# Kernel optimization log

Measured on AMD Instinct MI355X. Metric: run time of the kernel, lower is better.

The kernel has to match this reference:

```python
import jax, jax.numpy as jnp
import numpy as np

SCALE = 8.0  # sqrt(d_head=64)
NEG = -1e9


def setup_inputs() -> dict:
    key = jax.random.key(0)
    kq, kk, kv, km = jax.random.split(key, 4)
    B, H, S, D = 2, 16, 2048, 64
    q = jax.random.normal(kq, (B, H, S, D), dtype=jnp.float32)
    k = jax.random.normal(kk, (B, H, S, D), dtype=jnp.float32)
    v = jax.random.normal(kv, (B, H, S, D), dtype=jnp.float32)
    mask = jax.random.randint(km, (B, 1, 1, S), 0, 2, dtype=jnp.int32)
    return {"q": q, "k": k, "v": v, "mask": mask}


def reference(q, k, v, mask):
    # scores: [B,H,S,S]
    scores = jnp.einsum("bhqd,bhkd->bhqk", q / SCALE, k)
    scores = jnp.where(mask == 0, NEG, scores)
    attn = jax.nn.softmax(scores, axis=-1)  # dropout p=0 -> identity
    out = jnp.einsum("bhqk,bhkd->bhqd", attn, v)
    return (out, attn)
```

## Files before the change

### kernel.cpp

```cpp
#include <hip/hip_runtime.h>
#include <hip/hip_bf16.h>


#define S_LEN 2048
#define DH 64
#define QT 128
#define NCH (S_LEN / 64)

typedef __attribute__((ext_vector_type(8))) short  s16x8;
typedef __attribute__((ext_vector_type(4))) short  s16x4;
typedef __attribute__((ext_vector_type(8))) __bf16 bf16x8;
typedef __attribute__((ext_vector_type(4))) float  f32x4;
typedef __attribute__((ext_vector_type(2))) unsigned int u32x2;

__device__ __forceinline__ short f2bf(float x) {
    __hip_bfloat16 h = __float2bfloat16(x);
    return *reinterpret_cast<short*>(&h);
}
__device__ __forceinline__ unsigned pack2(float a, float b) {
    return (unsigned)(unsigned short)f2bf(a) | ((unsigned)(unsigned short)f2bf(b) << 16);
}
__device__ __forceinline__ bf16x8 ldfrag(const short* p) {
    s16x8 t = *(const s16x8*)p;
    return __builtin_bit_cast(bf16x8, t);
}
__device__ __forceinline__ int SW (int r, int c) { return r * 64 + (c ^ ((r & 7) << 3)); }
__device__ __forceinline__ int SWF(int r, int c) { return r * 64 + (c ^ ((r & 7) << 3)); }

__global__ __launch_bounds__(512, 4) void sdpa_kernel(
    const float* __restrict__ q, const float* __restrict__ k,
    const float* __restrict__ v, const int* __restrict__ mask,
    float* __restrict__ out, float* __restrict__ attn)
{
    __shared__ __align__(16) short shK[2][64 * 64];
    __shared__ __align__(16) short shVt[2][64 * 64];
    __shared__ __align__(16) float shPT[8][16 * 64];
    __shared__ char shMask[S_LEN];

    const int tid  = threadIdx.x;
    const int lane = tid & 63;
    const int w    = tid >> 6;
    const int l15  = lane & 15;
    const int lg   = lane >> 4;

    const int bh = blockIdx.y;
    const int q0 = blockIdx.x * QT;
    const int b  = bh >> 4;

    const float* qbase = q + ((size_t)bh * S_LEN + q0) * DH;
    const float* kbase = k + (size_t)bh * S_LEN * DH;
    const float* vbase = v + (size_t)bh * S_LEN * DH;
    float* attnbh = attn + (size_t)bh * S_LEN * S_LEN;

    for (int i = tid; i < S_LEN; i += 512)
        shMask[i] = (char)(mask[b * S_LEN + i] != 0);

    const int qrow = w * 16 + l15;
    bf16x8 qf0, qf1;
    {
        const float* qp = qbase + qrow * DH + 8 * lg;
        const float4 a0 = *(const float4*)(qp);
        const float4 a1 = *(const float4*)(qp + 4);
        const float4 b0 = *(const float4*)(qp + 32);
        const float4 b1 = *(const float4*)(qp + 36);
        s16x8 t0, t1;
        t0[0]=f2bf(a0.x*0.125f); t0[1]=f2bf(a0.y*0.125f); t0[2]=f2bf(a0.z*0.125f); t0[3]=f2bf(a0.w*0.125f);
        t0[4]=f2bf(a1.x*0.125f); t0[5]=f2bf(a1.y*0.125f); t0[6]=f2bf(a1.z*0.125f); t0[7]=f2bf(a1.w*0.125f);
        t1[0]=f2bf(b0.x*0.125f); t1[1]=f2bf(b0.y*0.125f); t1[2]=f2bf(b0.z*0.125f); t1[3]=f2bf(b0.w*0.125f);
        t1[4]=f2bf(b1.x*0.125f); t1[5]=f2bf(b1.y*0.125f); t1[6]=f2bf(b1.z*0.125f); t1[7]=f2bf(b1.w*0.125f);
        qf0 = __builtin_bit_cast(bf16x8, t0);
        qf1 = __builtin_bit_cast(bf16x8, t1);
    }

    const int krow = tid >> 3;
    const int kd0  = (tid & 7) * 8;
    auto loadK = [&](int c0, float4& a, float4& bb) {
        const float* src = kbase + (size_t)(c0 + krow) * DH + kd0;
        a  = *(const float4*)(src);
        bb = *(const float4*)(src + 4);
    };
    auto writeK = [&](short* dst, const float4& a, const float4& bb) {
        s16x8 vv;
        vv[0]=f2bf(a.x);  vv[1]=f2bf(a.y);  vv[2]=f2bf(a.z);  vv[3]=f2bf(a.w);
        vv[4]=f2bf(bb.x); vv[5]=f2bf(bb.y); vv[6]=f2bf(bb.z); vv[7]=f2bf(bb.w);
        *(s16x8*)&dst[SW(krow, kd0)] = vv;
    };
    const int vr0 = (tid & 31) * 2;
    const int vdg = tid >> 5;
    auto loadV = [&](int c0, float4& a, float4& bb) {
        const float* src = vbase + (size_t)(c0 + vr0) * DH + vdg * 4;
        a  = *(const float4*)(src);
        bb = *(const float4*)(src + DH);
    };
    auto writeVt = [&](short* dst, const float4& a, const float4& bb) {
        const float av[4] = {a.x, a.y, a.z, a.w};
        const float bv[4] = {bb.x, bb.y, bb.z, bb.w};
        int* dw = (int*)dst;
#pragma unroll
        for (int i = 0; i < 4; ++i) {
            const int d = vdg * 4 + i;
            dw[(d * 64 + (vr0 ^ ((d & 7) << 3))) >> 1] = (int)pack2(av[i], bv[i]);
        }
    };

    float4 ka, kb;
    loadK(0, ka, kb);
    writeK(shK[0], ka, kb);
    __syncthreads();

    float lacc = 0.f;
    for (int t = 0; t < NCH; ++t) {
        const int cur = t & 1;
        if (t + 1 < NCH) loadK((t + 1) * 64, ka, kb);
        __syncthreads();
        const short* K = shK[cur];
        const int c0 = t * 64;
        f32x4 s[4] = {{0,0,0,0},{0,0,0,0},{0,0,0,0},{0,0,0,0}};
#pragma unroll
        for (int ct = 0; ct < 4; ++ct) {
            const int kc = ct * 16 + l15;
            bf16x8 kf = ldfrag(&K[SW(kc, 8 * lg)]);
            s[ct] = __builtin_amdgcn_mfma_f32_16x16x32_bf16(kf, qf0, s[ct], 0, 0, 0);
            kf = ldfrag(&K[SW(kc, 32 + 8 * lg)]);
            s[ct] = __builtin_amdgcn_mfma_f32_16x16x32_bf16(kf, qf1, s[ct], 0, 0, 0);
        }
#pragma unroll
        for (int ct = 0; ct < 4; ++ct) {
            const unsigned mw = *(const unsigned*)&shMask[c0 + ct * 16 + lg * 4];
#pragma unroll
            for (int r = 0; r < 4; ++r)
                lacc += ((mw >> (8 * r)) & 1u) ? __expf(s[ct][r]) : 0.f;
        }
        if (t + 1 < NCH) writeK(shK[cur ^ 1], ka, kb);
    }
    lacc += __shfl_xor(lacc, 16);
    lacc += __shfl_xor(lacc, 32);
    const float lnInvl = -__logf(lacc);

    f32x4 oacc[4] = {{0,0,0,0},{0,0,0,0},{0,0,0,0},{0,0,0,0}};
    float4 va, vb;
    loadK(0, ka, kb);
    loadV(0, va, vb);
    writeK(shK[0], ka, kb);
    writeVt(shVt[0], va, vb);

    float* const shPTw = shPT[w];
    for (int t = 0; t < NCH; ++t) {
        const int cur = t & 1;
        if (t + 1 < NCH) { loadK((t + 1) * 64, ka, kb); loadV((t + 1) * 64, va, vb); }
        __syncthreads();
        const short* K  = shK[cur];
        const short* Vt = shVt[cur];
        const int c0 = t * 64;

        f32x4 s[4] = {{0,0,0,0},{0,0,0,0},{0,0,0,0},{0,0,0,0}};
#pragma unroll
        for (int ct = 0; ct < 4; ++ct) {
            const int kc = ct * 16 + l15;
            bf16x8 kf = ldfrag(&K[SW(kc, 8 * lg)]);
            s[ct] = __builtin_amdgcn_mfma_f32_16x16x32_bf16(kf, qf0, s[ct], 0, 0, 0);
            kf = ldfrag(&K[SW(kc, 32 + 8 * lg)]);
            s[ct] = __builtin_amdgcn_mfma_f32_16x16x32_bf16(kf, qf1, s[ct], 0, 0, 0);
        }
        s16x4 pf[4];
#pragma unroll
        for (int ct = 0; ct < 4; ++ct) {
            const unsigned mw = *(const unsigned*)&shMask[c0 + ct * 16 + lg * 4];
            f32x4 p;
#pragma unroll
            for (int r = 0; r < 4; ++r)
                p[r] = ((mw >> (8 * r)) & 1u) ? __expf(s[ct][r] + lnInvl) : 0.f;
            *(f32x4*)&shPTw[SWF(l15, ct * 16 + lg * 4)] = p;
            u32x2 pk;
            pk[0] = pack2(p[0], p[1]);
            pk[1] = pack2(p[2], p[3]);
            pf[ct] = __builtin_bit_cast(s16x4, pk);
        }
#pragma unroll
        for (int st = 0; st < 4; ++st) {
            const int rowIdx = (lane >> 3) + (st >> 1) * 8;
            const int cm     = (lane & 7) * 4 + (st & 1) * 32;
            const f32x4 pv_ = *(const f32x4*)&shPTw[SWF(rowIdx, cm)];
            __builtin_nontemporal_store(
                pv_, (f32x4*)(attnbh + (size_t)(q0 + w * 16 + rowIdx) * S_LEN + c0 + cm));
        }
#pragma unroll
        for (int dt = 0; dt < 4; ++dt) {
#pragma unroll
            for (int ct = 0; ct < 4; ++ct) {
                const s16x4 af = *(const s16x4*)&Vt[SW(dt * 16 + l15, ct * 16 + 4 * lg)];
                oacc[dt] = __builtin_amdgcn_mfma_f32_16x16x16bf16_1k(af, pf[ct], oacc[dt], 0, 0, 0);
            }
        }
        if (t + 1 < NCH) { writeK(shK[cur ^ 1], ka, kb); writeVt(shVt[cur ^ 1], va, vb); }
    }

    float* obase = out + ((size_t)bh * S_LEN + q0 + qrow) * DH;
#pragma unroll
    for (int dt = 0; dt < 4; ++dt)
        __builtin_nontemporal_store(oacc[dt], (f32x4*)(obase + dt * 16 + lg * 4));
}

extern "C" void kernel_launch(void* const* d_in, const int* in_sizes, int n_in,
                              void* d_out, int out_size, void* d_ws, size_t ws_size,
                              hipStream_t stream)
{
    const float* q    = (const float*)d_in[0];
    const float* k    = (const float*)d_in[1];
    const float* v    = (const float*)d_in[2];
    const int*   mask = (const int*)d_in[3];
    float* out  = (float*)d_out;
    float* attn = out + (size_t)2 * 16 * 2048 * 64;

    dim3 grid(S_LEN / QT, 2 * 16);
    sdpa_kernel<<<grid, dim3(512), 0, stream>>>(q, k, v, mask, out, attn);
}
```

Baseline: 168.5 us.

## Widen normalizer pass to 128-key chunks and reorder main-loop staging

The first pass, which computes the softmax denominator, now processes 128 keys per iteration. It uses wider K loads, four split accumulators and half as many barriers, with K kept in a shared-memory arena that the second pass also reuses. In the second pass, the next K/V tile is written to shared memory and the PV MFMAs are issued before the attention-matrix stores. This aims to overlap global stores with compute and to drop one barrier on the first iteration. The row sums are passed through shPT with an extra block barrier. The wider loads add register pressure under the 512-thread, 4-block launch bound.

```diff
diff --git a/kernel.cpp b/kernel.cpp
--- a/kernel.cpp
+++ b/kernel.cpp
@@ -6,6 +6,7 @@
 #define DH 64
 #define QT 128
 #define NCH (S_LEN / 64)
+#define NCHA (S_LEN / 128)
 
 typedef __attribute__((ext_vector_type(8))) short  s16x8;
 typedef __attribute__((ext_vector_type(4))) short  s16x4;
@@ -32,8 +33,7 @@
     const float* __restrict__ v, const int* __restrict__ mask,
     float* __restrict__ out, float* __restrict__ attn)
 {
-    __shared__ __align__(16) short shK[2][64 * 64];
-    __shared__ __align__(16) short shVt[2][64 * 64];
+    __shared__ __align__(16) char  arena[32 * 1024];
     __shared__ __align__(16) float shPT[8][16 * 64];
     __shared__ char shMask[S_LEN];
 
@@ -72,29 +72,90 @@
         qf1 = __builtin_bit_cast(bf16x8, t1);
     }
 
+    {
+        const int krow2 = tid >> 2;
+        const int kd2   = (tid & 3) * 16;
+        float4 k0_, k1_, k2_, k3_;
+        auto loadK2 = [&](int c0) {
+            const float* src = kbase + (size_t)(c0 + krow2) * DH + kd2;
+            k0_ = *(const float4*)(src);
+            k1_ = *(const float4*)(src + 4);
+            k2_ = *(const float4*)(src + 8);
+            k3_ = *(const float4*)(src + 12);
+        };
+        auto writeK2 = [&](short* dst) {
+            s16x8 v0, v1;
+            v0[0]=f2bf(k0_.x); v0[1]=f2bf(k0_.y); v0[2]=f2bf(k0_.z); v0[3]=f2bf(k0_.w);
+            v0[4]=f2bf(k1_.x); v0[5]=f2bf(k1_.y); v0[6]=f2bf(k1_.z); v0[7]=f2bf(k1_.w);
+            v1[0]=f2bf(k2_.x); v1[1]=f2bf(k2_.y); v1[2]=f2bf(k2_.z); v1[3]=f2bf(k2_.w);
+            v1[4]=f2bf(k3_.x); v1[5]=f2bf(k3_.y); v1[6]=f2bf(k3_.z); v1[7]=f2bf(k3_.w);
+            *(s16x8*)&dst[SW(krow2, kd2)]     = v0;
+            *(s16x8*)&dst[SW(krow2, kd2 + 8)] = v1;
+        };
+
+        loadK2(0);
+        writeK2((short*)arena);
+        __syncthreads();
+
+        float lacc4[4] = {0.f, 0.f, 0.f, 0.f};
+        for (int t = 0; t < NCHA; ++t) {
+            const int cur = t & 1;
+            if (t + 1 < NCHA) loadK2((t + 1) * 128);
+            __syncthreads();
+            const short* K = (const short*)(arena + cur * 16384);
+            const int c0 = t * 128;
+            f32x4 s[8] = {{0,0,0,0},{0,0,0,0},{0,0,0,0},{0,0,0,0},
+                          {0,0,0,0},{0,0,0,0},{0,0,0,0},{0,0,0,0}};
+#pragma unroll
+            for (int ct = 0; ct < 8; ++ct) {
+                const int kc = ct * 16 + l15;
+                bf16x8 kf = ldfrag(&K[SW(kc, 8 * lg)]);
+                s[ct] = __builtin_amdgcn_mfma_f32_16x16x32_bf16(kf, qf0, s[ct], 0, 0, 0);
+                kf = ldfrag(&K[SW(kc, 32 + 8 * lg)]);
+                s[ct] = __builtin_amdgcn_mfma_f32_16x16x32_bf16(kf, qf1, s[ct], 0, 0, 0);
+            }
+#pragma unroll
+            for (int ct = 0; ct < 8; ++ct) {
+                const unsigned mw = *(const unsigned*)&shMask[c0 + ct * 16 + lg * 4];
+#pragma unroll
+                for (int r = 0; r < 4; ++r)
+                    lacc4[ct & 3] += ((mw >> (8 * r)) & 1u) ? __expf(s[ct][r]) : 0.f;
+            }
+            if (t + 1 < NCHA) writeK2((short*)(arena + (cur ^ 1) * 16384));
+        }
+        float la = (lacc4[0] + lacc4[1]) + (lacc4[2] + lacc4[3]);
+        la += __shfl_xor(la, 16);
+        la += __shfl_xor(la, 32);
+        shPT[w][lane] = la;
+    }
+    __syncthreads();
+    const float lnInvl = -__logf(shPT[w][lane]);
+
     const int krow = tid >> 3;
     const int kd0  = (tid & 7) * 8;
-    auto loadK = [&](int c0, float4& a, float4& bb) {
+    float4 ka, kb;
+    auto loadK = [&](int c0) {
         const float* src = kbase + (size_t)(c0 + krow) * DH + kd0;
-        a  = *(const float4*)(src);
-        bb = *(const float4*)(src + 4);
-    };
-    auto writeK = [&](short* dst, const float4& a, const float4& bb) {
+        ka = *(const float4*)(src);
+        kb = *(const float4*)(src + 4);
+    };
+    auto writeK = [&](short* dst) {
         s16x8 vv;
-        vv[0]=f2bf(a.x);  vv[1]=f2bf(a.y);  vv[2]=f2bf(a.z);  vv[3]=f2bf(a.w);
-        vv[4]=f2bf(bb.x); vv[5]=f2bf(bb.y); vv[6]=f2bf(bb.z); vv[7]=f2bf(bb.w);
+        vv[0]=f2bf(ka.x); vv[1]=f2bf(ka.y); vv[2]=f2bf(ka.z); vv[3]=f2bf(ka.w);
+        vv[4]=f2bf(kb.x); vv[5]=f2bf(kb.y); vv[6]=f2bf(kb.z); vv[7]=f2bf(kb.w);
         *(s16x8*)&dst[SW(krow, kd0)] = vv;
     };
     const int vr0 = (tid & 31) * 2;
     const int vdg = tid >> 5;
-    auto loadV = [&](int c0, float4& a, float4& bb) {
+    float4 va, vb;
+    auto loadV = [&](int c0) {
         const float* src = vbase + (size_t)(c0 + vr0) * DH + vdg * 4;
-        a  = *(const float4*)(src);
-        bb = *(const float4*)(src + DH);
-    };
-    auto writeVt = [&](short* dst, const float4& a, const float4& bb) {
-        const float av[4] = {a.x, a.y, a.z, a.w};
-        const float bv[4] = {bb.x, bb.y, bb.z, bb.w};
+        va = *(const float4*)(src);
+        vb = *(const float4*)(src + DH);
+    };
+    auto writeVt = [&](short* dst) {
+        const float av[4] = {va.x, va.y, va.z, va.w};
+        const float bv[4] = {vb.x, vb.y, vb.z, vb.w};
         int* dw = (int*)dst;
 #pragma unroll
         for (int i = 0; i < 4; ++i) {
@@ -102,55 +163,23 @@
             dw[(d * 64 + (vr0 ^ ((d & 7) << 3))) >> 1] = (int)pack2(av[i], bv[i]);
         }
     };
-
-    float4 ka, kb;
-    loadK(0, ka, kb);
-    writeK(shK[0], ka, kb);
+    auto KB  = [&](int cur) -> short* { return (short*)arena + cur * 4096; };
+    auto VTB = [&](int cur) -> short* { return (short*)(arena + 16384) + cur * 4096; };
+
+    f32x4 oacc[4] = {{0,0,0,0},{0,0,0,0},{0,0,0,0},{0,0,0,0}};
+    loadK(0);
+    loadV(0);
+    writeK(KB(0));
+    writeVt(VTB(0));
     __syncthreads();
-
-    float lacc = 0.f;
-    for (int t = 0; t < NCH; ++t) {
-        const int cur = t & 1;
-        if (t + 1 < NCH) loadK((t + 1) * 64, ka, kb);
-        __syncthreads();
-        const short* K = shK[cur];
-        const int c0 = t * 64;
-        f32x4 s[4] = {{0,0,0,0},{0,0,0,0},{0,0,0,0},{0,0,0,0}};
-#pragma unroll
-        for (int ct = 0; ct < 4; ++ct) {
-            const int kc = ct * 16 + l15;
-            bf16x8 kf = ldfrag(&K[SW(kc, 8 * lg)]);
-            s[ct] = __builtin_amdgcn_mfma_f32_16x16x32_bf16(kf, qf0, s[ct], 0, 0, 0);
-            kf = ldfrag(&K[SW(kc, 32 + 8 * lg)]);
-            s[ct] = __builtin_amdgcn_mfma_f32_16x16x32_bf16(kf, qf1, s[ct], 0, 0, 0);
-        }
-#pragma unroll
-        for (int ct = 0; ct < 4; ++ct) {
-            const unsigned mw = *(const unsigned*)&shMask[c0 + ct * 16 + lg * 4];
-#pragma unroll
-            for (int r = 0; r < 4; ++r)
-                lacc += ((mw >> (8 * r)) & 1u) ? __expf(s[ct][r]) : 0.f;
-        }
-        if (t + 1 < NCH) writeK(shK[cur ^ 1], ka, kb);
-    }
-    lacc += __shfl_xor(lacc, 16);
-    lacc += __shfl_xor(lacc, 32);
-    const float lnInvl = -__logf(lacc);
-
-    f32x4 oacc[4] = {{0,0,0,0},{0,0,0,0},{0,0,0,0},{0,0,0,0}};
-    float4 va, vb;
-    loadK(0, ka, kb);
-    loadV(0, va, vb);
-    writeK(shK[0], ka, kb);
-    writeVt(shVt[0], va, vb);
 
     float* const shPTw = shPT[w];
     for (int t = 0; t < NCH; ++t) {
         const int cur = t & 1;
-        if (t + 1 < NCH) { loadK((t + 1) * 64, ka, kb); loadV((t + 1) * 64, va, vb); }
-        __syncthreads();
-        const short* K  = shK[cur];
-        const short* Vt = shVt[cur];
+        if (t + 1 < NCH) { loadK((t + 1) * 64); loadV((t + 1) * 64); }
+        if (t > 0) __syncthreads();
+        const short* K  = KB(cur);
+        const short* Vt = VTB(cur);
         const int c0 = t * 64;
 
         f32x4 s[4] = {{0,0,0,0},{0,0,0,0},{0,0,0,0},{0,0,0,0}};
@@ -176,6 +205,15 @@
             pk[1] = pack2(p[2], p[3]);
             pf[ct] = __builtin_bit_cast(s16x4, pk);
         }
+        if (t + 1 < NCH) { writeK(KB(cur ^ 1)); writeVt(VTB(cur ^ 1)); }
+#pragma unroll
+        for (int dt = 0; dt < 4; ++dt) {
+#pragma unroll
+            for (int ct = 0; ct < 4; ++ct) {
+                const s16x4 af = *(const s16x4*)&Vt[SW(dt * 16 + l15, ct * 16 + 4 * lg)];
+                oacc[dt] = __builtin_amdgcn_mfma_f32_16x16x16bf16_1k(af, pf[ct], oacc[dt], 0, 0, 0);
+            }
+        }
 #pragma unroll
         for (int st = 0; st < 4; ++st) {
             const int rowIdx = (lane >> 3) + (st >> 1) * 8;
@@ -184,15 +222,6 @@
             __builtin_nontemporal_store(
                 pv_, (f32x4*)(attnbh + (size_t)(q0 + w * 16 + rowIdx) * S_LEN + c0 + cm));
         }
-#pragma unroll
-        for (int dt = 0; dt < 4; ++dt) {
-#pragma unroll
-            for (int ct = 0; ct < 4; ++ct) {
-                const s16x4 af = *(const s16x4*)&Vt[SW(dt * 16 + l15, ct * 16 + 4 * lg)];
-                oacc[dt] = __builtin_amdgcn_mfma_f32_16x16x16bf16_1k(af, pf[ct], oacc[dt], 0, 0, 0);
-            }
-        }
-        if (t + 1 < NCH) { writeK(shK[cur ^ 1], ka, kb); writeVt(shVt[cur ^ 1], va, vb); }
     }
 
     float* obase = out + ((size_t)bh * S_LEN + q0 + qrow) * DH;
```

Measured after the change: 171.1 us. Within noise of the previous version (+1.6%).

## Precompute swizzled bf16 K and transposed V tiles in a prep kernel

Applied to the files above, without the earlier changes.

Adds a prep kernel that converts K to bf16 and V to transposed bf16 once, writing them into workspace already in the swizzled shared-memory layout. The main kernel then copies each 8 KB chunk to LDS with one 16-byte load and store per thread. This removes the repeated fp32 loads, conversions and scattered transposed LDS writes that every query block did three times per chunk, and halves the global K/V bytes read. The cost is an extra launch plus a workspace write and read. A fallback keeps the old kernel when the workspace is too small.

```diff
diff --git a/kernel.cpp b/kernel.cpp
--- a/kernel.cpp
+++ b/kernel.cpp
@@ -27,13 +27,65 @@
 __device__ __forceinline__ int SW (int r, int c) { return r * 64 + (c ^ ((r & 7) << 3)); }
 __device__ __forceinline__ int SWF(int r, int c) { return r * 64 + (c ^ ((r & 7) << 3)); }
 
-__global__ __launch_bounds__(512, 4) void sdpa_kernel(
-    const float* __restrict__ q, const float* __restrict__ k,
-    const float* __restrict__ v, const int* __restrict__ mask,
+__global__ __launch_bounds__(256, 4) void prep_kernel(
+    const float* __restrict__ k, const float* __restrict__ v,
+    short* __restrict__ wsK, short* __restrict__ wsVt)
+{
+    __shared__ float tile[64 * 65];
+    const int tid = threadIdx.x;
+    const int blk = blockIdx.x;
+    const int bh = blk >> 5;
+    const int c  = blk & 31;
+
+    const float* kc = k + (((size_t)bh * S_LEN) + c * 64) * DH;
+    const float* vc = v + (((size_t)bh * S_LEN) + c * 64) * DH;
+    short* dstK = wsK  + ((size_t)bh * 32 + c) * 4096;
+    short* dstV = wsVt + ((size_t)bh * 32 + c) * 4096;
+
+    const int r  = tid >> 2;
+    const int d0 = (tid & 3) * 16;
+    {
+        const float* src = kc + r * DH + d0;
+        const float4 a0 = *(const float4*)(src);
+        const float4 a1 = *(const float4*)(src + 4);
+        const float4 a2 = *(const float4*)(src + 8);
+        const float4 a3 = *(const float4*)(src + 12);
+        s16x8 v0, v1;
+        v0[0]=f2bf(a0.x); v0[1]=f2bf(a0.y); v0[2]=f2bf(a0.z); v0[3]=f2bf(a0.w);
+        v0[4]=f2bf(a1.x); v0[5]=f2bf(a1.y); v0[6]=f2bf(a1.z); v0[7]=f2bf(a1.w);
+        v1[0]=f2bf(a2.x); v1[1]=f2bf(a2.y); v1[2]=f2bf(a2.z); v1[3]=f2bf(a2.w);
+        v1[4]=f2bf(a3.x); v1[5]=f2bf(a3.y); v1[6]=f2bf(a3.z); v1[7]=f2bf(a3.w);
+        *(s16x8*)&dstK[SW(r, d0)]     = v0;
+        *(s16x8*)&dstK[SW(r, d0 + 8)] = v1;
+    }
+    {
+        const float* src = vc + r * DH + d0;
+        *(float4*)&tile[r * 65 + d0]      = *(const float4*)(src);
+        *(float4*)&tile[r * 65 + d0 + 4]  = *(const float4*)(src + 4);
+        *(float4*)&tile[r * 65 + d0 + 8]  = *(const float4*)(src + 8);
+        *(float4*)&tile[r * 65 + d0 + 12] = *(const float4*)(src + 12);
+    }
+    __syncthreads();
+    {
+        const int d  = tid >> 2;
+        const int kb = (tid & 3) * 16;
+        s16x8 w0, w1;
+#pragma unroll
+        for (int i = 0; i < 8; ++i) w0[i] = f2bf(tile[(kb + i) * 65 + d]);
+#pragma unroll
+        for (int i = 0; i < 8; ++i) w1[i] = f2bf(tile[(kb + 8 + i) * 65 + d]);
+        *(s16x8*)&dstV[SW(d, kb)]     = w0;
+        *(s16x8*)&dstV[SW(d, kb + 8)] = w1;
+    }
+}
+
+__global__ __launch_bounds__(512, 4) void sdpa_main(
+    const float* __restrict__ q, const short* __restrict__ wsK,
+    const short* __restrict__ wsVt, const int* __restrict__ mask,
     float* __restrict__ out, float* __restrict__ attn)
 {
-    __shared__ __align__(16) short shK[2][64 * 64];
-    __shared__ __align__(16) short shVt[2][64 * 64];
+    __shared__ __align__(16) short shK[2][4096];
+    __shared__ __align__(16) short shVt[2][4096];
     __shared__ __align__(16) float shPT[8][16 * 64];
     __shared__ char shMask[S_LEN];
 
@@ -48,8 +100,8 @@
     const int b  = bh >> 4;
 
     const float* qbase = q + ((size_t)bh * S_LEN + q0) * DH;
-    const float* kbase = k + (size_t)bh * S_LEN * DH;
-    const float* vbase = v + (size_t)bh * S_LEN * DH;
+    const short* wsKbh = wsK  + (size_t)bh * 32 * 4096;
+    const short* wsVbh = wsVt + (size_t)bh * 32 * 4096;
     float* attnbh = attn + (size_t)bh * S_LEN * S_LEN;
 
     for (int i = tid; i < S_LEN; i += 512)
@@ -72,46 +124,20 @@
         qf1 = __builtin_bit_cast(bf16x8, t1);
     }
 
-    const int krow = tid >> 3;
-    const int kd0  = (tid & 7) * 8;
-    auto loadK = [&](int c0, float4& a, float4& bb) {
-        const float* src = kbase + (size_t)(c0 + krow) * DH + kd0;
-        a  = *(const float4*)(src);
-        bb = *(const float4*)(src + 4);
-    };
-    auto writeK = [&](short* dst, const float4& a, const float4& bb) {
-        s16x8 vv;
-        vv[0]=f2bf(a.x);  vv[1]=f2bf(a.y);  vv[2]=f2bf(a.z);  vv[3]=f2bf(a.w);
-        vv[4]=f2bf(bb.x); vv[5]=f2bf(bb.y); vv[6]=f2bf(bb.z); vv[7]=f2bf(bb.w);
-        *(s16x8*)&dst[SW(krow, kd0)] = vv;
-    };
-    const int vr0 = (tid & 31) * 2;
-    const int vdg = tid >> 5;
-    auto loadV = [&](int c0, float4& a, float4& bb) {
-        const float* src = vbase + (size_t)(c0 + vr0) * DH + vdg * 4;
-        a  = *(const float4*)(src);
-        bb = *(const float4*)(src + DH);
-    };
-    auto writeVt = [&](short* dst, const float4& a, const float4& bb) {
-        const float av[4] = {a.x, a.y, a.z, a.w};
-        const float bv[4] = {bb.x, bb.y, bb.z, bb.w};
-        int* dw = (int*)dst;
-#pragma unroll
-        for (int i = 0; i < 4; ++i) {
-            const int d = vdg * 4 + i;
-            dw[(d * 64 + (vr0 ^ ((d & 7) << 3))) >> 1] = (int)pack2(av[i], bv[i]);
-        }
-    };
-
-    float4 ka, kb;
-    loadK(0, ka, kb);
-    writeK(shK[0], ka, kb);
+    s16x8 kreg, vreg;
+    auto loadKc = [&](int c) { kreg = *(const s16x8*)(wsKbh + (size_t)c * 4096 + tid * 8); };
+    auto loadVc = [&](int c) { vreg = *(const s16x8*)(wsVbh + (size_t)c * 4096 + tid * 8); };
+    auto putK = [&](int buf) { *(s16x8*)&shK[buf][tid * 8] = kreg; };
+    auto putV = [&](int buf) { *(s16x8*)&shVt[buf][tid * 8] = vreg; };
+
+    loadKc(0);
+    putK(0);
     __syncthreads();
 
     float lacc = 0.f;
     for (int t = 0; t < NCH; ++t) {
         const int cur = t & 1;
-        if (t + 1 < NCH) loadK((t + 1) * 64, ka, kb);
+        if (t + 1 < NCH) loadKc(t + 1);
         __syncthreads();
         const short* K = shK[cur];
         const int c0 = t * 64;
@@ -131,23 +157,22 @@
             for (int r = 0; r < 4; ++r)
                 lacc += ((mw >> (8 * r)) & 1u) ? __expf(s[ct][r]) : 0.f;
         }
-        if (t + 1 < NCH) writeK(shK[cur ^ 1], ka, kb);
+        if (t + 1 < NCH) putK(cur ^ 1);
     }
     lacc += __shfl_xor(lacc, 16);
     lacc += __shfl_xor(lacc, 32);
     const float lnInvl = -__logf(lacc);
 
     f32x4 oacc[4] = {{0,0,0,0},{0,0,0,0},{0,0,0,0},{0,0,0,0}};
-    float4 va, vb;
-    loadK(0, ka, kb);
-    loadV(0, va, vb);
-    writeK(shK[0], ka, kb);
-    writeVt(shVt[0], va, vb);
+    loadKc(0);
+    loadVc(0);
+    putK(0);
+    putV(0);
 
     float* const shPTw = shPT[w];
     for (int t = 0; t < NCH; ++t) {
         const int cur = t & 1;
-        if (t + 1 < NCH) { loadK((t + 1) * 64, ka, kb); loadV((t + 1) * 64, va, vb); }
+        if (t + 1 < NCH) { loadKc(t + 1); loadVc(t + 1); }
         __syncthreads();
         const short* K  = shK[cur];
         const short* Vt = shVt[cur];
@@ -192,7 +217,181 @@
                 oacc[dt] = __builtin_amdgcn_mfma_f32_16x16x16bf16_1k(af, pf[ct], oacc[dt], 0, 0, 0);
             }
         }
-        if (t + 1 < NCH) { writeK(shK[cur ^ 1], ka, kb); writeVt(shVt[cur ^ 1], va, vb); }
+        if (t + 1 < NCH) { putK(cur ^ 1); putV(cur ^ 1); }
+    }
+
+    float* obase = out + ((size_t)bh * S_LEN + q0 + qrow) * DH;
+#pragma unroll
+    for (int dt = 0; dt < 4; ++dt)
+        __builtin_nontemporal_store(oacc[dt], (f32x4*)(obase + dt * 16 + lg * 4));
+}
+
+__global__ __launch_bounds__(512, 4) void sdpa_fallback(
+    const float* __restrict__ q, const float* __restrict__ k,
+    const float* __restrict__ v, const int* __restrict__ mask,
+    float* __restrict__ out, float* __restrict__ attn)
+{
+    __shared__ __align__(16) short shK[2][64 * 64];
+    __shared__ __align__(16) short shVt[2][64 * 64];
+    __shared__ __align__(16) float shPT[8][16 * 64];
+    __shared__ char shMask[S_LEN];
+
+    const int tid  = threadIdx.x;
+    const int lane = tid & 63;
+    const int w    = tid >> 6;
+    const int l15  = lane & 15;
+    const int lg   = lane >> 4;
+
+    const int bh = blockIdx.y;
+    const int q0 = blockIdx.x * QT;
+    const int b  = bh >> 4;
+
+    const float* qbase = q + ((size_t)bh * S_LEN + q0) * DH;
+    const float* kbase = k + (size_t)bh * S_LEN * DH;
+    const float* vbase = v + (size_t)bh * S_LEN * DH;
+    float* attnbh = attn + (size_t)bh * S_LEN * S_LEN;
+
+    for (int i = tid; i < S_LEN; i += 512)
+        shMask[i] = (char)(mask[b * S_LEN + i] != 0);
+
+    const int qrow = w * 16 + l15;
+    bf16x8 qf0, qf1;
+    {
+        const float* qp = qbase + qrow * DH + 8 * lg;
+        const float4 a0 = *(const float4*)(qp);
+        const float4 a1 = *(const float4*)(qp + 4);
+        const float4 b0 = *(const float4*)(qp + 32);
+        const float4 b1 = *(const float4*)(qp + 36);
+        s16x8 t0, t1;
+        t0[0]=f2bf(a0.x*0.125f); t0[1]=f2bf(a0.y*0.125f); t0[2]=f2bf(a0.z*0.125f); t0[3]=f2bf(a0.w*0.125f);
+        t0[4]=f2bf(a1.x*0.125f); t0[5]=f2bf(a1.y*0.125f); t0[6]=f2bf(a1.z*0.125f); t0[7]=f2bf(a1.w*0.125f);
+        t1[0]=f2bf(b0.x*0.125f); t1[1]=f2bf(b0.y*0.125f); t1[2]=f2bf(b0.z*0.125f); t1[3]=f2bf(b0.w*0.125f);
+        t1[4]=f2bf(b1.x*0.125f); t1[5]=f2bf(b1.y*0.125f); t1[6]=f2bf(b1.z*0.125f); t1[7]=f2bf(b1.w*0.125f);
+        qf0 = __builtin_bit_cast(bf16x8, t0);
+        qf1 = __builtin_bit_cast(bf16x8, t1);
+    }
+
+    const int krow = tid >> 3;
+    const int kd0  = (tid & 7) * 8;
+    float4 ka, kb;
+    auto loadK = [&](int c0) {
+        const float* src = kbase + (size_t)(c0 + krow) * DH + kd0;
+        ka = *(const float4*)(src);
+        kb = *(const float4*)(src + 4);
+    };
+    auto writeK = [&](short* dst) {
+        s16x8 vv;
+        vv[0]=f2bf(ka.x); vv[1]=f2bf(ka.y); vv[2]=f2bf(ka.z); vv[3]=f2bf(ka.w);
+        vv[4]=f2bf(kb.x); vv[5]=f2bf(kb.y); vv[6]=f2bf(kb.z); vv[7]=f2bf(kb.w);
+        *(s16x8*)&dst[SW(krow, kd0)] = vv;
+    };
+    const int vr0 = (tid & 31) * 2;
+    const int vdg = tid >> 5;
+    float4 va, vb;
+    auto loadV = [&](int c0) {
+        const float* src = vbase + (size_t)(c0 + vr0) * DH + vdg * 4;
+        va = *(const float4*)(src);
+        vb = *(const float4*)(src + DH);
+    };
+    auto writeVt = [&](short* dst) {
+        const float av[4] = {va.x, va.y, va.z, va.w};
+        const float bv[4] = {vb.x, vb.y, vb.z, vb.w};
+        int* dw = (int*)dst;
+#pragma unroll
+        for (int i = 0; i < 4; ++i) {
+            const int d = vdg * 4 + i;
+            dw[(d * 64 + (vr0 ^ ((d & 7) << 3))) >> 1] = (int)pack2(av[i], bv[i]);
+        }
+    };
+
+    loadK(0);
+    writeK(shK[0]);
+    __syncthreads();
+
+    float lacc = 0.f;
+    for (int t = 0; t < NCH; ++t) {
+        const int cur = t & 1;
+        if (t + 1 < NCH) loadK((t + 1) * 64);
+        __syncthreads();
+        const short* K = shK[cur];
+        const int c0 = t * 64;
+        f32x4 s[4] = {{0,0,0,0},{0,0,0,0},{0,0,0,0},{0,0,0,0}};
+#pragma unroll
+        for (int ct = 0; ct < 4; ++ct) {
+            const int kc = ct * 16 + l15;
+            bf16x8 kf = ldfrag(&K[SW(kc, 8 * lg)]);
+            s[ct] = __builtin_amdgcn_mfma_f32_16x16x32_bf16(kf, qf0, s[ct], 0, 0, 0);
+            kf = ldfrag(&K[SW(kc, 32 + 8 * lg)]);
+            s[ct] = __builtin_amdgcn_mfma_f32_16x16x32_bf16(kf, qf1, s[ct], 0, 0, 0);
+        }
+#pragma unroll
+        for (int ct = 0; ct < 4; ++ct) {
+            const unsigned mw = *(const unsigned*)&shMask[c0 + ct * 16 + lg * 4];
+#pragma unroll
+            for (int r = 0; r < 4; ++r)
+                lacc += ((mw >> (8 * r)) & 1u) ? __expf(s[ct][r]) : 0.f;
+        }
+        if (t + 1 < NCH) writeK(shK[cur ^ 1]);
+    }
+    lacc += __shfl_xor(lacc, 16);
+    lacc += __shfl_xor(lacc, 32);
+    const float lnInvl = -__logf(lacc);
+
+    f32x4 oacc[4] = {{0,0,0,0},{0,0,0,0},{0,0,0,0},{0,0,0,0}};
+    loadK(0);
+    loadV(0);
+    writeK(shK[0]);
+    writeVt(shVt[0]);
+
+    float* const shPTw = shPT[w];
+    for (int t = 0; t < NCH; ++t) {
+        const int cur = t & 1;
+        if (t + 1 < NCH) { loadK((t + 1) * 64); loadV((t + 1) * 64); }
+        __syncthreads();
+        const short* K  = shK[cur];
+        const short* Vt = shVt[cur];
+        const int c0 = t * 64;
+
+        f32x4 s[4] = {{0,0,0,0},{0,0,0,0},{0,0,0,0},{0,0,0,0}};
+#pragma unroll
+        for (int ct = 0; ct < 4; ++ct) {
+            const int kc = ct * 16 + l15;
+            bf16x8 kf = ldfrag(&K[SW(kc, 8 * lg)]);
+            s[ct] = __builtin_amdgcn_mfma_f32_16x16x32_bf16(kf, qf0, s[ct], 0, 0, 0);
+            kf = ldfrag(&K[SW(kc, 32 + 8 * lg)]);
+            s[ct] = __builtin_amdgcn_mfma_f32_16x16x32_bf16(kf, qf1, s[ct], 0, 0, 0);
+        }
+        s16x4 pf[4];
+#pragma unroll
+        for (int ct = 0; ct < 4; ++ct) {
+            const unsigned mw = *(const unsigned*)&shMask[c0 + ct * 16 + lg * 4];
+            f32x4 p;
+#pragma unroll
+            for (int r = 0; r < 4; ++r)
+                p[r] = ((mw >> (8 * r)) & 1u) ? __expf(s[ct][r] + lnInvl) : 0.f;
+            *(f32x4*)&shPTw[SWF(l15, ct * 16 + lg * 4)] = p;
+            u32x2 pk;
+            pk[0] = pack2(p[0], p[1]);
+            pk[1] = pack2(p[2], p[3]);
+            pf[ct] = __builtin_bit_cast(s16x4, pk);
+        }
+#pragma unroll
+        for (int st = 0; st < 4; ++st) {
+            const int rowIdx = (lane >> 3) + (st >> 1) * 8;
+            const int cm     = (lane & 7) * 4 + (st & 1) * 32;
+            const f32x4 pv_ = *(const f32x4*)&shPTw[SWF(rowIdx, cm)];
+            __builtin_nontemporal_store(
+                pv_, (f32x4*)(attnbh + (size_t)(q0 + w * 16 + rowIdx) * S_LEN + c0 + cm));
+        }
+#pragma unroll
+        for (int dt = 0; dt < 4; ++dt) {
+#pragma unroll
+            for (int ct = 0; ct < 4; ++ct) {
+                const s16x4 af = *(const s16x4*)&Vt[SW(dt * 16 + l15, ct * 16 + 4 * lg)];
+                oacc[dt] = __builtin_amdgcn_mfma_f32_16x16x16bf16_1k(af, pf[ct], oacc[dt], 0, 0, 0);
+            }
+        }
+        if (t + 1 < NCH) { writeK(shK[cur ^ 1]); writeVt(shVt[cur ^ 1]); }
     }
 
     float* obase = out + ((size_t)bh * S_LEN + q0 + qrow) * DH;
@@ -212,6 +411,15 @@
     float* out  = (float*)d_out;
     float* attn = out + (size_t)2 * 16 * 2048 * 64;
 
+    const size_t WS_NEED = (size_t)2 * 32 * 32 * 4096 * sizeof(short);
     dim3 grid(S_LEN / QT, 2 * 16);
-    sdpa_kernel<<<grid, dim3(512), 0, stream>>>(q, k, v, mask, out, attn);
-}
+
+    if (ws_size >= WS_NEED) {
+        short* wsK  = (short*)d_ws;
+        short* wsVt = wsK + (size_t)32 * 32 * 4096;
+        prep_kernel<<<dim3(1024), dim3(256), 0, stream>>>(k, v, wsK, wsVt);
+        sdpa_main<<<grid, dim3(512), 0, stream>>>(q, wsK, wsVt, mask, out, attn);
+    } else {
+        sdpa_fallback<<<grid, dim3(512), 0, stream>>>(q, k, v, mask, out, attn);
+    }
+}
```

Measured after the change: 181.2 us. 7.6% more time.
